# Performance work log

Measured on AMD Instinct MI355X. Metric: run time of the kernel, lower is better.

The kernel has to match this reference:

```python
import jax, jax.numpy as jnp
import numpy as np
import math

B, T, N, D = 8, 4, 2048, 256
M, E = 4096, 8

def setup_inputs() -> dict:
    key = jax.random.key(0)
    ks = jax.random.split(key, 8)
    std = 0.02
    return {
        "prop_embed": jax.random.normal(ks[0], (B, T, N, D), jnp.float32),
        "adap_embed": jax.random.normal(ks[1], (B, N, D), jnp.float32),
        "x_proj_w": jax.random.normal(ks[2], (D, D), jnp.float32) * (1.0 / np.sqrt(D)),
        "x_proj_b": jnp.zeros((D,), jnp.float32),
        "keyMatrix": jax.random.normal(ks[3], (M, D), jnp.float32) * std,
        "memMatrix": jax.random.normal(ks[4], (M, D), jnp.float32) * std,
        "w_gate": jax.random.normal(ks[5], (D, E), jnp.float32) * (1.0 / np.sqrt(D)),
        "w_noise": jax.random.normal(ks[6], (D, E), jnp.float32) * (1.0 / np.sqrt(D)),
    }

def reference(prop_embed, adap_embed, x_proj_w, x_proj_b, keyMatrix, memMatrix, w_gate, w_noise):
    b, t, n, d = prop_embed.shape
    m = memMatrix.shape[0]
    x = jnp.mean(prop_embed, axis=1)                      # [B,N,D]
    q = jnp.tanh(x @ x_proj_w.T + x_proj_b)               # [B,N,D]
    att = jnp.einsum('bnd,md->bnm', q, keyMatrix)         # [B,N,M]
    # eval mode: noise_stddev * self.training == 0, so noisy_logits == clean_logits
    clean_logits = memMatrix @ w_gate                     # [M,E]
    mem_label = jax.nn.softmax(clean_logits, axis=-1)     # [M,E]
    # sparse_qk: keep top-k = int(ln(M)) logits, rest -> -inf
    k = int(math.log(m))
    vals, idx = jax.lax.top_k(att, k)                     # [B,N,k]
    att2 = jnp.full((b * n, m), -jnp.inf, dtype=att.dtype)
    rows = jnp.arange(b * n)[:, None]
    att2 = att2.at[rows, idx.reshape(b * n, k)].set(vals.reshape(b * n, k))
    att_w = jax.nn.softmax(att2, axis=-1).reshape(b, n, m)
    mem_retrieved = jnp.einsum('bnm,md->bnd', att_w, memMatrix)
    label_retrieved = jnp.einsum('bnm,me->bne', att_w, mem_label)
    gate = label_retrieved
    return (gate, mem_retrieved, label_retrieved, mem_label, att_w)
```

## Files before the change

### kernel.cpp

```cpp
#include <hip/hip_runtime.h>
#include <hip/hip_fp16.h>
#include <math.h>

#define Bb 8
#define Tt 4
#define Nn 2048
#define Dd 256
#define Mm 4096
#define Ee 8
#define ROWS (Bb*Nn)
#define KSEL 8
#define KC 16

#define O_GATE 0LL
#define O_MEMR 131072LL
#define O_LABR 4325376LL
#define O_MLAB 4456448LL
#define O_ATTW 4489216LL

#define WS_WT    0LL
#define WS_KH    262144LL
#define WS_T16P  2359296LL
#define WS_T16I  3407872LL

typedef float f32x4 __attribute__((ext_vector_type(4)));
typedef short short8 __attribute__((ext_vector_type(8)));
typedef _Float16 f16x8 __attribute__((ext_vector_type(8)));

__device__ __forceinline__ unsigned short f2h(float x) {
    __half h = __float2half(x);
    return *reinterpret_cast<unsigned short*>(&h);
}

__device__ __forceinline__ void gload_lds16(const void* g, void* l) {
    __builtin_amdgcn_global_load_lds(
        (const __attribute__((address_space(1))) unsigned int*)g,
        (__attribute__((address_space(3))) unsigned int*)l,
        16, 0, 0);
}

__global__ void k_transpose(const float* __restrict__ W, float* __restrict__ WT) {
    int i = blockIdx.x * 256 + threadIdx.x;
    int r = i >> 8, c = i & 255;
    WT[c * 256 + r] = W[r * 256 + c];
}

__global__ __launch_bounds__(256) void k_q(const float* __restrict__ prop,
                                           const float* __restrict__ WT,
                                           const float* __restrict__ bias,
                                           float* __restrict__ qf,
                                           unsigned short* __restrict__ qh) {
    __shared__ float xs[16][256];
    int tid = threadIdx.x;
    int row0 = blockIdx.x * 16;
    #pragma unroll
    for (int r = 0; r < 16; ++r) {
        int row = row0 + r;
        int b = row >> 11;
        int n = row & 2047;
        const float* p = prop + ((long long)(b * Tt) * Nn + n) * Dd + tid;
        float s = 0.f;
        #pragma unroll
        for (int t = 0; t < Tt; ++t) s += p[(long long)t * Nn * Dd];
        xs[r][tid] = s * 0.25f;
    }
    __syncthreads();
    float acc[16];
    #pragma unroll
    for (int r = 0; r < 16; ++r) acc[r] = 0.f;
    int c = tid;
    for (int d = 0; d < 256; ++d) {
        float wv = WT[d * 256 + c];
        #pragma unroll
        for (int r = 0; r < 16; ++r) acc[r] = fmaf(xs[r][d], wv, acc[r]);
    }
    float bv = bias[c];
    #pragma unroll
    for (int r = 0; r < 16; ++r) {
        float qv = tanhf(acc[r] + bv);
        long long o = (long long)(row0 + r) * Dd + c;
        qf[o] = qv;
        qh[o] = f2h(qv);
    }
}

__global__ void k_key16(const float* __restrict__ key, unsigned short* __restrict__ kh) {
    int idx = blockIdx.x * 256 + threadIdx.x;
    kh[idx] = f2h(key[idx]);
}

__global__ __launch_bounds__(256) void k_mlabel(const float* __restrict__ mem,
                                                const float* __restrict__ wg,
                                                float* __restrict__ mlab) {
    int m = blockIdx.x * 256 + threadIdx.x;
    if (m >= Mm) return;
    float acc[Ee];
    #pragma unroll
    for (int e = 0; e < Ee; ++e) acc[e] = 0.f;
    const float* mr = mem + (long long)m * Dd;
    for (int d = 0; d < Dd; ++d) {
        float mv = mr[d];
        #pragma unroll
        for (int e = 0; e < Ee; ++e) acc[e] = fmaf(mv, wg[d * Ee + e], acc[e]);
    }
    float mx = acc[0];
    #pragma unroll
    for (int e = 1; e < Ee; ++e) mx = fmaxf(mx, acc[e]);
    float z = 0.f;
    #pragma unroll
    for (int e = 0; e < Ee; ++e) { acc[e] = expf(acc[e] - mx); z += acc[e]; }
    float inv = 1.f / z;
    #pragma unroll
    for (int e = 0; e < Ee; ++e) mlab[(long long)m * Ee + e] = acc[e] * inv;
}

__global__ __launch_bounds__(256) void k_att(const unsigned short* __restrict__ qh,
                                             const unsigned short* __restrict__ kh,
                                             unsigned short* __restrict__ attH) {
    __shared__ __align__(16) unsigned short smem[8192];
    int tid = threadIdx.x;
    int lane = tid & 63, w = tid >> 6;
    int wr = w >> 1, wc = w & 1;
    long long row0 = (long long)blockIdx.y * 128;
    long long col0 = (long long)blockIdx.x * 128;

    f32x4 acc[4][4];
    #pragma unroll
    for (int m = 0; m < 4; ++m)
        #pragma unroll
        for (int n = 0; n < 4; ++n) acc[m][n] = (f32x4){0.f, 0.f, 0.f, 0.f};

    int rr = lane >> 2;
    int sp = lane & 3;

    auto stage = [&](int k0) {
        #pragma unroll
        for (int t = 0; t < 2; ++t) {
            const unsigned short* src = t ? kh : qh;
            long long b0 = t ? col0 : row0;
            #pragma unroll
            for (int i = 0; i < 2; ++i) {
                int r = w * 32 + i * 16 + rr;
                int sl = sp ^ ((r >> 1) & 3);
                const unsigned short* g = src + (b0 + r) * 256 + k0 * 32 + sl * 8;
                unsigned short* l = smem + t * 4096 + (w * 32 + i * 16) * 32;
                gload_lds16(g, l);
            }
        }
    };

    stage(0);
    for (int k0 = 0; k0 < 8; ++k0) {
        __syncthreads();
        int lr = lane & 15, j = lane >> 4;
        f16x8 ah[4], bh[4];
        #pragma unroll
        for (int m = 0; m < 4; ++m) {
            int r = wr * 64 + m * 16 + lr;
            int off = r * 32 + ((j ^ ((r >> 1) & 3)) * 8);
            ah[m] = *(const f16x8*)(smem + off);
        }
        #pragma unroll
        for (int n = 0; n < 4; ++n) {
            int r = wc * 64 + n * 16 + lr;
            int off = r * 32 + ((j ^ ((r >> 1) & 3)) * 8);
            bh[n] = *(const f16x8*)(smem + 4096 + off);
        }
        #pragma unroll
        for (int m = 0; m < 4; ++m)
            #pragma unroll
            for (int n = 0; n < 4; ++n)
                acc[m][n] = __builtin_amdgcn_mfma_f32_16x16x32_f16(ah[m], bh[n], acc[m][n], 0, 0, 0);
        if (k0 < 7) { __syncthreads(); stage(k0 + 1); }
    }

    int lr = lane & 15, j = lane >> 4;
    #pragma unroll
    for (int m = 0; m < 4; ++m)
        #pragma unroll
        for (int n = 0; n < 4; ++n) {
            long long C = col0 + wc * 64 + n * 16 + lr;
            #pragma unroll
            for (int reg = 0; reg < 4; ++reg) {
                long long R = row0 + wr * 64 + m * 16 + j * 4 + reg;
                attH[R * Mm + C] = f2h(acc[m][n][reg]);
            }
        }
}

__global__ __launch_bounds__(256) void k_final2(const unsigned short* __restrict__ attH,
                                                const float* __restrict__ qf,
                                                const float* __restrict__ key,
                                                const float* __restrict__ mem,
                                                const float* __restrict__ mlab,
                                                float* __restrict__ gate,
                                                float* __restrict__ memr,
                                                float* __restrict__ labr,
                                                float* __restrict__ t16p,
                                                int* __restrict__ t16i) {
    int tid = threadIdx.x;
    int lane = tid & 63;
    long long row = (long long)blockIdx.x * 4 + (tid >> 6);
    const unsigned short* arow = attH + row * Mm;

    unsigned int v[8];
    #pragma unroll
    for (int s = 0; s < 8; ++s) v[s] = 0u;

    #pragma unroll
    for (int t = 0; t < 8; ++t) {
        int c8 = t * 64 + lane;
        short8 x8 = *(const short8*)(arow + c8 * 8);
        unsigned int rb = (unsigned)(4095 - c8 * 8);
        #pragma unroll
        for (int jj = 0; jj < 8; ++jj) {
            unsigned int b = (unsigned short)x8[jj];
            unsigned int sr = (unsigned)((int)(b << 16) >> 31);
            unsigned int mono = b ^ ((sr >> 17) | 0x8000u);
            unsigned int keyv = (mono << 16) | (rb - jj);
            if (keyv > v[7]) {
                unsigned int x = keyv;
                #pragma unroll
                for (int s = 0; s < 8; ++s) {
                    unsigned int hi = v[s] > x ? v[s] : x;
                    unsigned int lo = v[s] > x ? x : v[s];
                    v[s] = hi; x = lo;
                }
            }
        }
    }

    unsigned int sk[KC];
    #pragma unroll
    for (int k = 0; k < KC; ++k) {
        unsigned int bv = v[0];
        #pragma unroll
        for (int d = 1; d < 64; d <<= 1) {
            unsigned int ov = (unsigned)__shfl_xor((int)bv, d);
            bv = bv > ov ? bv : ov;
        }
        sk[k] = bv;
        bool won = (v[0] == bv);
        #pragma unroll
        for (int s = 0; s < 7; ++s) v[s] = won ? v[s + 1] : v[s];
        v[7] = won ? 0u : v[7];
    }

    int civ[KC];
    #pragma unroll
    for (int s = 0; s < KC; ++s) civ[s] = 4095 - (int)(sk[s] & 0xFFFFu);

    int c = lane & 15, g = lane >> 4;
    int cidx = civ[0];
    #pragma unroll
    for (int s = 1; s < KC; ++s) cidx = (c == s) ? civ[s] : cidx;
    const float* qrow = qf + row * Dd;
    const float* krow = key + (long long)cidx * Dd;
    double dacc = 0.0;
    #pragma unroll
    for (int i = 0; i < 16; ++i) {
        float4 qv = *(const float4*)(qrow + g * 64 + i * 4);
        float4 kv = *(const float4*)(krow + g * 64 + i * 4);
        dacc = fma((double)qv.x, (double)kv.x, dacc);
        dacc = fma((double)qv.y, (double)kv.y, dacc);
        dacc = fma((double)qv.z, (double)kv.z, dacc);
        dacc = fma((double)qv.w, (double)kv.w, dacc);
    }
    dacc += __shfl_xor(dacc, 16);
    dacc += __shfl_xor(dacc, 32);
    float rvf = (float)dacc;

    float cv[KC];
    #pragma unroll
    for (int s = 0; s < KC; ++s) cv[s] = __shfl(rvf, s);

    unsigned int m32[KC];
    #pragma unroll
    for (int s = 0; s < KC; ++s) {
        unsigned int fb = __float_as_uint(cv[s]);
        m32[s] = fb ^ ((unsigned)((int)fb >> 31) | 0x80000000u);
    }
    bool sel[KC];
    #pragma unroll
    for (int s = 0; s < KC; ++s) {
        int r = 0;
        #pragma unroll
        for (int t = 0; t < KC; ++t) {
            if (t != s) {
                bool gt = (m32[t] > m32[s]) || (m32[t] == m32[s] && civ[t] < civ[s]);
                r += gt ? 1 : 0;
            }
        }
        sel[s] = (r < KSEL);
    }

    float mx = cv[0];
    #pragma unroll
    for (int s = 1; s < KC; ++s) mx = fmaxf(mx, cv[s]);
    float p[KC]; float z = 0.f;
    #pragma unroll
    for (int s = 0; s < KC; ++s) { p[s] = sel[s] ? expf(cv[s] - mx) : 0.f; z += p[s]; }
    float inv = 1.f / z;
    #pragma unroll
    for (int s = 0; s < KC; ++s) p[s] *= inv;

    {
        float4 a = make_float4(0.f, 0.f, 0.f, 0.f);
        #pragma unroll
        for (int s = 0; s < KC; ++s) {
            if (sel[s]) {
                const float4 mv = *(const float4*)(mem + (long long)civ[s] * Dd + lane * 4);
                a.x = fmaf(p[s], mv.x, a.x); a.y = fmaf(p[s], mv.y, a.y);
                a.z = fmaf(p[s], mv.z, a.z); a.w = fmaf(p[s], mv.w, a.w);
            }
        }
        *(float4*)(memr + row * Dd + lane * 4) = a;
    }

    if (lane < Ee) {
        float s8 = 0.f;
        #pragma unroll
        for (int s = 0; s < KC; ++s)
            if (sel[s]) s8 = fmaf(p[s], mlab[(long long)civ[s] * Ee + lane], s8);
        gate[row * Ee + lane] = s8;
        labr[row * Ee + lane] = s8;
    }
    if (lane < KC) {
        float myp = p[0]; int myi = civ[0];
        #pragma unroll
        for (int s = 1; s < KC; ++s) {
            myp = (lane == s) ? p[s] : myp;
            myi = (lane == s) ? civ[s] : myi;
        }
        t16p[row * KC + lane] = myp;
        t16i[row * KC + lane] = myi;
    }
}

__global__ __launch_bounds__(256) void k_attw(const float* __restrict__ t16p,
                                              const int* __restrict__ t16i,
                                              float* __restrict__ attw) {
    int tid = threadIdx.x, lane = tid & 63;
    long long row = (long long)blockIdx.x * 4 + (tid >> 6);
    float* arow = attw + row * Mm;
    float4 zz = make_float4(0.f, 0.f, 0.f, 0.f);
    #pragma unroll
    for (int t = 0; t < 16; ++t)
        *(float4*)(arow + (t * 64 + lane) * 4) = zz;
    __syncthreads();
    if (lane < KC) {
        float pv = t16p[row * KC + lane];
        int iv = t16i[row * KC + lane];
        arow[iv] = pv;
    }
}

extern "C" void kernel_launch(void* const* d_in, const int* in_sizes, int n_in,
                              void* d_out, int out_size, void* d_ws, size_t ws_size,
                              hipStream_t stream) {
    const float* prop = (const float*)d_in[0];
    const float* W    = (const float*)d_in[2];
    const float* bias = (const float*)d_in[3];
    const float* key  = (const float*)d_in[4];
    const float* mem  = (const float*)d_in[5];
    const float* wg   = (const float*)d_in[6];

    float* out  = (float*)d_out;
    float* gate = out + O_GATE;
    float* memr = out + O_MEMR;
    float* labr = out + O_LABR;
    float* mlab = out + O_MLAB;
    float* attw = out + O_ATTW;

    char* ws = (char*)d_ws;
    float*          WT   = (float*)(ws + WS_WT);
    unsigned short* kh   = (unsigned short*)(ws + WS_KH);
    float*          t16p = (float*)(ws + WS_T16P);
    int*            t16i = (int*)(ws + WS_T16I);

    unsigned short* attH = (unsigned short*)attw;
    unsigned short* qh   = attH + (long long)ROWS * Mm;
    float*          qf   = memr;

    k_transpose<<<256, 256, 0, stream>>>(W, WT);
    k_q<<<ROWS / 16, 256, 0, stream>>>(prop, WT, bias, qf, qh);
    k_key16<<<(Mm * Dd) / 256, 256, 0, stream>>>(key, kh);
    k_mlabel<<<Mm / 256, 256, 0, stream>>>(mem, wg, mlab);
    dim3 g2(Mm / 128, ROWS / 128);
    k_att<<<g2, 256, 0, stream>>>(qh, kh, attH);
    k_final2<<<ROWS / 4, 256, 0, stream>>>(attH, qf, key, mem, mlab, gate, memr, labr, t16p, t16i);
    k_attw<<<ROWS / 4, 256, 0, stream>>>(t16p, t16i, attw);
}
```

Measured before the change: 307.3 us.

## Fuse att_w scatter into final kernel, move fp16 scratch to workspace, swizzle GEMM blocks

Removes the separate k_attw kernel. k_final2 now zeroes its own att_w row with nontemporal stores and scatters the top-k probabilities directly, so the t16p/t16i round trip through global memory goes away. The fp16 attention matrix and q buffer move from the output region into the workspace, which lets the output be written while attH is still being read. The attention GEMM now uses a 1D grid with a block-index swizzle to change cache locality across XCDs. The risk is that the workspace must be large enough for attH and qH.

```diff
diff --git a/kernel.cpp b/kernel.cpp
--- a/kernel.cpp
+++ b/kernel.cpp
@@ -20,8 +20,8 @@
 
 #define WS_WT    0LL
 #define WS_KH    262144LL
-#define WS_T16P  2359296LL
-#define WS_T16I  3407872LL
+#define WS_ATTH  16777216LL
+#define WS_QH    150994944LL
 
 typedef float f32x4 __attribute__((ext_vector_type(4)));
 typedef short short8 __attribute__((ext_vector_type(8)));
@@ -118,11 +118,15 @@
                                              const unsigned short* __restrict__ kh,
                                              unsigned short* __restrict__ attH) {
     __shared__ __align__(16) unsigned short smem[8192];
+    int bid = blockIdx.x;
+    int swz = (bid & 7) * 512 + (bid >> 3);
+    int bx = swz & 31;
+    int by = swz >> 5;
     int tid = threadIdx.x;
     int lane = tid & 63, w = tid >> 6;
     int wr = w >> 1, wc = w & 1;
-    long long row0 = (long long)blockIdx.y * 128;
-    long long col0 = (long long)blockIdx.x * 128;
+    long long row0 = (long long)by * 128;
+    long long col0 = (long long)bx * 128;
 
     f32x4 acc[4][4];
     #pragma unroll
@@ -196,8 +200,7 @@
                                                 float* __restrict__ gate,
                                                 float* __restrict__ memr,
                                                 float* __restrict__ labr,
-                                                float* __restrict__ t16p,
-                                                int* __restrict__ t16i) {
+                                                float* __restrict__ attw) {
     int tid = threadIdx.x;
     int lane = tid & 63;
     long long row = (long long)blockIdx.x * 4 + (tid >> 6);
@@ -325,6 +328,15 @@
         gate[row * Ee + lane] = s8;
         labr[row * Ee + lane] = s8;
     }
+
+    float* awrow = attw + row * Mm;
+    {
+        f32x4 zz = (f32x4){0.f, 0.f, 0.f, 0.f};
+        #pragma unroll
+        for (int t = 0; t < 16; ++t)
+            __builtin_nontemporal_store(zz, (f32x4*)(awrow + (t * 64 + lane) * 4));
+    }
+    __syncthreads();
     if (lane < KC) {
         float myp = p[0]; int myi = civ[0];
         #pragma unroll
@@ -332,26 +344,7 @@
             myp = (lane == s) ? p[s] : myp;
             myi = (lane == s) ? civ[s] : myi;
         }
-        t16p[row * KC + lane] = myp;
-        t16i[row * KC + lane] = myi;
-    }
-}
-
-__global__ __launch_bounds__(256) void k_attw(const float* __restrict__ t16p,
-                                              const int* __restrict__ t16i,
-                                              float* __restrict__ attw) {
-    int tid = threadIdx.x, lane = tid & 63;
-    long long row = (long long)blockIdx.x * 4 + (tid >> 6);
-    float* arow = attw + row * Mm;
-    float4 zz = make_float4(0.f, 0.f, 0.f, 0.f);
-    #pragma unroll
-    for (int t = 0; t < 16; ++t)
-        *(float4*)(arow + (t * 64 + lane) * 4) = zz;
-    __syncthreads();
-    if (lane < KC) {
-        float pv = t16p[row * KC + lane];
-        int iv = t16i[row * KC + lane];
-        arow[iv] = pv;
+        awrow[myi] = myp;
     }
 }
 
@@ -375,19 +368,14 @@
     char* ws = (char*)d_ws;
     float*          WT   = (float*)(ws + WS_WT);
     unsigned short* kh   = (unsigned short*)(ws + WS_KH);
-    float*          t16p = (float*)(ws + WS_T16P);
-    int*            t16i = (int*)(ws + WS_T16I);
-
-    unsigned short* attH = (unsigned short*)attw;
-    unsigned short* qh   = attH + (long long)ROWS * Mm;
+    unsigned short* attH = (unsigned short*)(ws + WS_ATTH);
+    unsigned short* qh   = (unsigned short*)(ws + WS_QH);
     float*          qf   = memr;
 
     k_transpose<<<256, 256, 0, stream>>>(W, WT);
     k_q<<<ROWS / 16, 256, 0, stream>>>(prop, WT, bias, qf, qh);
     k_key16<<<(Mm * Dd) / 256, 256, 0, stream>>>(key, kh);
     k_mlabel<<<Mm / 256, 256, 0, stream>>>(mem, wg, mlab);
-    dim3 g2(Mm / 128, ROWS / 128);
-    k_att<<<g2, 256, 0, stream>>>(qh, kh, attH);
-    k_final2<<<ROWS / 4, 256, 0, stream>>>(attH, qf, key, mem, mlab, gate, memr, labr, t16p, t16i);
-    k_attw<<<ROWS / 4, 256, 0, stream>>>(t16p, t16i, attw);
-}
+    k_att<<<4096, 256, 0, stream>>>(qh, kh, attH);
+    k_final2<<<ROWS / 4, 256, 0, stream>>>(attH, qf, key, mem, mlab, gate, memr, labr, attw);
+}
```

Measured after the change: 276.3 us. 1.11x faster.
